# Kernel optimization log

Measured on AMD Instinct MI355X. Metric: run time of the kernel, lower is better.

## Reference

```python
import jax, jax.numpy as jnp
import numpy as np

D_MODEL = 512
N_HEADS = 8
D_HEAD = D_MODEL // N_HEADS
SCALE = D_HEAD ** -0.5


def _rel_shift(x):
    # x: (b, h, qlen, klen) -> Transformer-XL relative shift
    b, h, qlen, klen = x.shape
    x = jnp.pad(x, ((0, 0), (0, 0), (0, 0), (1, 0)))        # (b,h,q,k+1)
    x = x.reshape(b, h, klen + 1, qlen)
    x = x[:, :, 1:, :].reshape(b, h, qlen, klen)
    return x


def setup_inputs() -> dict:
    key = jax.random.key(0)
    ks = jax.random.split(key, 12)
    B, S = 2, 2048
    P = 2 * S - 1
    w = lambda k, shape: (jax.random.normal(k, shape, jnp.float32) * 0.02)
    return {
        "x": jax.random.normal(ks[0], (B, S, D_MODEL), jnp.float32),
        "pos_emb": jax.random.normal(ks[1], (P, D_MODEL), jnp.float32),
        "Wq": w(ks[2], (D_MODEL, D_MODEL)), "bq": jnp.zeros((D_MODEL,), jnp.float32),
        "Wk": w(ks[3], (D_MODEL, D_MODEL)), "bk": jnp.zeros((D_MODEL,), jnp.float32),
        "Wv": w(ks[4], (D_MODEL, D_MODEL)), "bv": jnp.zeros((D_MODEL,), jnp.float32),
        "Wp": w(ks[5], (D_MODEL, D_MODEL)),
        "Wo": w(ks[6], (D_MODEL, D_MODEL)), "bo": jnp.zeros((D_MODEL,), jnp.float32),
        "pos_bias_u": w(ks[7], (N_HEADS, D_HEAD)),
        "pos_bias_v": w(ks[8], (N_HEADS, D_HEAD)),
    }


def reference(x, pos_emb, Wq, bq, Wk, bk, Wv, bv, Wp, Wo, bo, pos_bias_u, pos_bias_v):
    B, S, _ = x.shape
    # projections (torch Linear: y = x @ W^T + b; here W stored as (in, out))
    q = (x @ Wq + bq).reshape(B, S, N_HEADS, D_HEAD)
    k = (x @ Wk + bk).reshape(B, S, N_HEADS, D_HEAD)
    v = (x @ Wv + bv).reshape(B, S, N_HEADS, D_HEAD)
    p = (pos_emb @ Wp).reshape(-1, N_HEADS, D_HEAD)  # (2S-1, H, D)

    # content score: (q + u) @ k^T  -> (B,H,S,S)
    content = jnp.einsum("bshd,bthd->bhst", q + pos_bias_u, k)
    # position score: (q + v_bias) @ p^T -> (B,H,S,2S-1), then rel_shift
    pos = jnp.einsum("bshd,phd->bhsp", q + pos_bias_v, p)
    pos = _rel_shift(pos)[..., :S]  # trim to kv_len

    attn = jax.nn.softmax((content + pos) * SCALE, axis=-1)
    out = jnp.einsum("bhst,bthd->bshd", attn, v).reshape(B, S, D_MODEL)
    out = out @ Wo + bo
    return out
```

## Files before the change

### kernel.cpp

```cpp
#include <hip/hip_runtime.h>

#define DM    512
#define NH    8
#define DH    64
#define SEQ   2048
#define PLEN  4095
#define NB    2
#define NSPLIT 2
#define JSPAN (SEQ / NSPLIT)
#define ATT_SCALE 0.125f

typedef __attribute__((ext_vector_type(8))) _Float16 half8;
typedef __attribute__((ext_vector_type(4))) float   floatx4;

__global__ __launch_bounds__(256)
void prep(const float* __restrict__ x, const float* __restrict__ pe,
          const float* __restrict__ W0, const float* __restrict__ W1,
          const float* __restrict__ W2, const float* __restrict__ W3,
          const float* __restrict__ W4,
          _Float16* __restrict__ x16, _Float16* __restrict__ pe16,
          _Float16* __restrict__ Wt)
{
    __shared__ _Float16 tile[64 * 72];
    const int z = blockIdx.z;
    const int t = threadIdx.x;

    if (z < 2) {
        const float* src = z ? pe : x;
        _Float16* dst = z ? pe16 : x16;
        const long n = z ? (long)PLEN * DM : (long)NB * SEQ * DM;
        const long i = ((long)blockIdx.x * 256 + t) * 8;
        if (i >= n) return;
        float4 f0 = *(const float4*)(src + i);
        float4 f1 = *(const float4*)(src + i + 4);
        half8 o;
        o[0] = (_Float16)f0.x; o[1] = (_Float16)f0.y;
        o[2] = (_Float16)f0.z; o[3] = (_Float16)f0.w;
        o[4] = (_Float16)f1.x; o[5] = (_Float16)f1.y;
        o[6] = (_Float16)f1.z; o[7] = (_Float16)f1.w;
        *(half8*)(dst + i) = o;
        return;
    }
    if (blockIdx.x >= 64) return;
    const int wz = z - 2;
    const float* W = (wz == 0) ? W0 : (wz == 1) ? W1 : (wz == 2) ? W2
                   : (wz == 3) ? W3 : W4;
    _Float16* dst_base = Wt + (size_t)wz * DM * DM;
    const int n0 = (blockIdx.x & 7) * 64, k0 = (blockIdx.x >> 3) * 64;
    {
        const int kr = t >> 2, nch = (t & 3) * 16;
        const float* src = W + (size_t)(k0 + kr) * DM + n0 + nch;
        float4 f0 = *(const float4*)(src + 0);
        float4 f1 = *(const float4*)(src + 4);
        float4 f2 = *(const float4*)(src + 8);
        float4 f3 = *(const float4*)(src + 12);
        _Float16* trow = &tile[kr * 72 + nch];
        trow[0]  = (_Float16)f0.x; trow[1]  = (_Float16)f0.y;
        trow[2]  = (_Float16)f0.z; trow[3]  = (_Float16)f0.w;
        trow[4]  = (_Float16)f1.x; trow[5]  = (_Float16)f1.y;
        trow[6]  = (_Float16)f1.z; trow[7]  = (_Float16)f1.w;
        trow[8]  = (_Float16)f2.x; trow[9]  = (_Float16)f2.y;
        trow[10] = (_Float16)f2.z; trow[11] = (_Float16)f2.w;
        trow[12] = (_Float16)f3.x; trow[13] = (_Float16)f3.y;
        trow[14] = (_Float16)f3.z; trow[15] = (_Float16)f3.w;
    }
    __syncthreads();
    {
        const int nr = t >> 2, kch = (t & 3) * 16;
        half8 o0, o1;
#pragma unroll
        for (int i = 0; i < 8; ++i) o0[i] = tile[(kch + i) * 72 + nr];
#pragma unroll
        for (int i = 0; i < 8; ++i) o1[i] = tile[(kch + 8 + i) * 72 + nr];
        _Float16* dst = dst_base + (size_t)(n0 + nr) * DM + k0 + kch;
        *(half8*)dst = o0;
        *(half8*)(dst + 8) = o1;
    }
}

__global__ __launch_bounds__(256)
void gemm_qkvp(const _Float16* __restrict__ X, const _Float16* __restrict__ Pe,
               const _Float16* __restrict__ Wt,
               const float* __restrict__ bq, const float* __restrict__ bk,
               const float* __restrict__ bv, const float* __restrict__ bu,
               const float* __restrict__ bvb,
               _Float16* __restrict__ qu16, _Float16* __restrict__ qv16,
               _Float16* __restrict__ k16, _Float16* __restrict__ vt16,
               _Float16* __restrict__ p16)
{
    __shared__ _Float16 aS[64 * 72];
    __shared__ _Float16 wS[64 * 72];

    const int t = threadIdx.x;
    const int w = t >> 6, lane = t & 63, quad = lane >> 4, l16 = lane & 15;
    const int z = blockIdx.z;
    const int n0 = blockIdx.x * 64;
    const int m0 = blockIdx.y * 64;
    const int srow = t >> 2, sch = (t & 3) * 16;
    const _Float16* A = (z == 3) ? Pe : X;
    const _Float16* Wz = Wt + (size_t)z * DM * DM;

    floatx4 acc[4];
#pragma unroll
    for (int ct = 0; ct < 4; ++ct) acc[ct] = (floatx4){0.f, 0.f, 0.f, 0.f};

    for (int k0 = 0; k0 < DM; k0 += 64) {
        __syncthreads();
        if (z != 3 || m0 + srow < PLEN) {
            const _Float16* asrc = A + (size_t)(m0 + srow) * DM + k0 + sch;
            *(half8*)&aS[srow * 72 + sch]     = *(const half8*)asrc;
            *(half8*)&aS[srow * 72 + sch + 8] = *(const half8*)(asrc + 8);
        } else {
            half8 zz = {};
            *(half8*)&aS[srow * 72 + sch]     = zz;
            *(half8*)&aS[srow * 72 + sch + 8] = zz;
        }
        {
            const _Float16* wsrc = Wz + (size_t)(n0 + srow) * DM + k0 + sch;
            *(half8*)&wS[srow * 72 + sch]     = *(const half8*)wsrc;
            *(half8*)&wS[srow * 72 + sch + 8] = *(const half8*)(wsrc + 8);
        }
        __syncthreads();
#pragma unroll
        for (int kb = 0; kb < 2; ++kb) {
            half8 af = *(const half8*)&aS[(16 * w + l16) * 72 + kb * 32 + quad * 8];
#pragma unroll
            for (int ct = 0; ct < 4; ++ct) {
                half8 bf = *(const half8*)&wS[(16 * ct + l16) * 72 + kb * 32 + quad * 8];
                acc[ct] = __builtin_amdgcn_mfma_f32_16x16x32_f16(af, bf, acc[ct], 0, 0, 0);
            }
        }
    }

    const int h = n0 >> 6;
    if (z == 0) {
#pragma unroll
        for (int ct = 0; ct < 4; ++ct) {
            const int n = n0 + 16 * ct + l16;
            const float bval = bq[n], uval = bu[n], vval = bvb[n];
#pragma unroll
            for (int r = 0; r < 4; ++r) {
                const int m = m0 + 16 * w + 4 * quad + r;
                const int b = m >> 11, s = m & 2047;
                const size_t dst = ((size_t)((h * NB + b) * SEQ) + s) * DH + (n & 63);
                const float q = acc[ct][r] + bval;
                qu16[dst] = (_Float16)((q + uval) * ATT_SCALE);
                qv16[dst] = (_Float16)((q + vval) * ATT_SCALE);
            }
        }
    } else if (z == 1) {
#pragma unroll
        for (int ct = 0; ct < 4; ++ct) {
            const int n = n0 + 16 * ct + l16;
            const float bval = bk[n];
#pragma unroll
            for (int r = 0; r < 4; ++r) {
                const int m = m0 + 16 * w + 4 * quad + r;
                const int b = m >> 11, s = m & 2047;
                k16[((size_t)((h * NB + b) * SEQ) + s) * DH + (n & 63)] =
                    (_Float16)(acc[ct][r] + bval);
            }
        }
    } else if (z == 2) {
        __syncthreads();
#pragma unroll
        for (int ct = 0; ct < 4; ++ct) {
            const float bval = bv[n0 + 16 * ct + l16];
#pragma unroll
            for (int r = 0; r < 4; ++r)
                aS[(16 * w + 4 * quad + r) * 72 + 16 * ct + l16] =
                    (_Float16)(acc[ct][r] + bval);
        }
        __syncthreads();
        const int b = m0 >> 11, s0 = m0 & 2047;
        const int drow = t >> 2;
        half8 o0, o1;
#pragma unroll
        for (int i = 0; i < 8; ++i) o0[i] = aS[(sch + i) * 72 + drow];
#pragma unroll
        for (int i = 0; i < 8; ++i) o1[i] = aS[(sch + 8 + i) * 72 + drow];
        _Float16* dst = vt16 + ((size_t)((h * NB + b) * DH) + drow) * SEQ + s0 + sch;
        *(half8*)dst = o0;
        *(half8*)(dst + 8) = o1;
    } else {
#pragma unroll
        for (int ct = 0; ct < 4; ++ct) {
            const int n = n0 + 16 * ct + l16;
#pragma unroll
            for (int r = 0; r < 4; ++r) {
                const int m = m0 + 16 * w + 4 * quad + r;
                if (m < PLEN)
                    p16[((size_t)h * PLEN + m) * DH + (n & 63)] = (_Float16)acc[ct][r];
            }
        }
    }
}

__global__ __launch_bounds__(256, 3)
void relattn_mfma(const _Float16* __restrict__ QU,
                  const _Float16* __restrict__ QV,
                  const _Float16* __restrict__ Kp,
                  const _Float16* __restrict__ VT,
                  const _Float16* __restrict__ Pp,
                  float* __restrict__ Opart, float* __restrict__ Lpart)
{
    __shared__ _Float16 kS[64 * 72];
    __shared__ _Float16 pS[128 * 72];
    __shared__ _Float16 vS[64 * 72];
    __shared__ _Float16 tS[64 * 88];

    const int t = threadIdx.x;
    const int w = t >> 6, lane = t & 63, quad = lane >> 4, l16 = lane & 15;
    const int i0 = blockIdx.x * 64;
    const int h = blockIdx.y;
    const int b = blockIdx.z & (NB - 1);
    const int split = blockIdx.z >> 1;
    const size_t hb = (size_t)(h * NB + b);
    const int cbase = 48 - 16 * w;

    half8 qa[2], va[2];
    {
        const _Float16* qrow = QU + (hb * SEQ + i0 + 16 * w + l16) * DH + quad * 8;
        const _Float16* vrow = QV + (hb * SEQ + i0 + 16 * w + l16) * DH + quad * 8;
        qa[0] = *(const half8*)qrow;       qa[1] = *(const half8*)(qrow + 32);
        va[0] = *(const half8*)vrow;       va[1] = *(const half8*)(vrow + 32);
    }

    floatx4 O[4];
    float lsum[4] = {0.f, 0.f, 0.f, 0.f};
#pragma unroll
    for (int ct = 0; ct < 4; ++ct) O[ct] = (floatx4){0.f, 0.f, 0.f, 0.f};

    const int srow = t >> 2, schunk = (t & 3) * 16;
    const int prow = t >> 1, pch = (t & 1) * 32;

    const _Float16* Kbase = Kp + hb * SEQ * DH;
    const _Float16* Vbase = VT + hb * DH * SEQ;
    const _Float16* Pbase = Pp + (size_t)h * PLEN * DH;

    const int jbeg = split * JSPAN, jend = jbeg + JSPAN;
    for (int j0 = jbeg; j0 < jend; j0 += 64) {
        __syncthreads();

        {
            const _Float16* src = Kbase + (size_t)(j0 + srow) * DH + schunk;
            half8 a0 = *(const half8*)src;
            half8 a1 = *(const half8*)(src + 8);
            *(half8*)&kS[srow * 72 + schunk] = a0;
            *(half8*)&kS[srow * 72 + schunk + 8] = a1;
            const _Float16* vsrc = Vbase + (size_t)srow * SEQ + j0 + schunk;
            half8 b0 = *(const half8*)vsrc;
            half8 b1 = *(const half8*)(vsrc + 8);
            *(half8*)&vS[srow * 72 + schunk] = b0;
            *(half8*)&vS[srow * 72 + schunk + 8] = b1;
        }
        {
            const int rbase = (SEQ - 1) + j0 - i0 - 63;
            if (prow < 127) {
                const _Float16* psrc = Pbase + (size_t)(rbase + prow) * DH + pch;
                half8 p0 = *(const half8*)(psrc + 0);
                half8 p1 = *(const half8*)(psrc + 8);
                half8 p2 = *(const half8*)(psrc + 16);
                half8 p3 = *(const half8*)(psrc + 24);
                *(half8*)&pS[prow * 72 + pch + 0]  = p0;
                *(half8*)&pS[prow * 72 + pch + 8]  = p1;
                *(half8*)&pS[prow * 72 + pch + 16] = p2;
                *(half8*)&pS[prow * 72 + pch + 24] = p3;
            }
        }
        __syncthreads();

        floatx4 Tacc[5], Sc[4];
#pragma unroll
        for (int c2 = 0; c2 < 5; ++c2) Tacc[c2] = (floatx4){0.f, 0.f, 0.f, 0.f};
#pragma unroll
        for (int ct = 0; ct < 4; ++ct) Sc[ct] = (floatx4){0.f, 0.f, 0.f, 0.f};
#pragma unroll
        for (int kb = 0; kb < 2; ++kb) {
#pragma unroll
            for (int c2 = 0; c2 < 5; ++c2) {
                half8 bf = *(const half8*)&pS[(cbase + 16 * c2 + l16) * 72 + kb * 32 + quad * 8];
                Tacc[c2] = __builtin_amdgcn_mfma_f32_16x16x32_f16(va[kb], bf, Tacc[c2], 0, 0, 0);
            }
#pragma unroll
            for (int ct = 0; ct < 4; ++ct) {
                half8 bf = *(const half8*)&kS[(16 * ct + l16) * 72 + kb * 32 + quad * 8];
                Sc[ct] = __builtin_amdgcn_mfma_f32_16x16x32_f16(qa[kb], bf, Sc[ct], 0, 0, 0);
            }
        }
#pragma unroll
        for (int c2 = 0; c2 < 5; ++c2)
#pragma unroll
            for (int r = 0; r < 4; ++r)
                tS[(16 * w + 4 * quad + r) * 88 + 16 * c2 + l16] = (_Float16)Tacc[c2][r];
        asm volatile("" ::: "memory");

#pragma unroll
        for (int ct = 0; ct < 4; ++ct)
#pragma unroll
            for (int r = 0; r < 4; ++r) {
                const int il16 = 4 * quad + r;
                const int c = 16 * ct + l16 - il16 + 15;
                const float e = __expf(Sc[ct][r] +
                                       (float)tS[(16 * w + il16) * 88 + c]);
                Sc[ct][r] = e;
                lsum[r] += e;
            }
        asm volatile("" ::: "memory");

#pragma unroll
        for (int ct = 0; ct < 4; ++ct)
#pragma unroll
            for (int r = 0; r < 4; ++r)
                tS[(16 * w + 4 * quad + r) * 88 + 16 * ct + l16] = (_Float16)Sc[ct][r];
        asm volatile("" ::: "memory");

#pragma unroll
        for (int kb = 0; kb < 2; ++kb) {
            half8 af = *(const half8*)&tS[(16 * w + l16) * 88 + kb * 32 + quad * 8];
#pragma unroll
            for (int ct = 0; ct < 4; ++ct) {
                half8 bf = *(const half8*)&vS[(16 * ct + l16) * 72 + kb * 32 + quad * 8];
                O[ct] = __builtin_amdgcn_mfma_f32_16x16x32_f16(af, bf, O[ct], 0, 0, 0);
            }
        }
        asm volatile("" ::: "memory");
    }

#pragma unroll
    for (int r = 0; r < 4; ++r) {
#pragma unroll
        for (int m = 1; m < 16; m <<= 1) lsum[r] += __shfl_xor(lsum[r], m);
        const int row = i0 + 16 * w + 4 * quad + r;
        float* orow = Opart + ((size_t)split * NB * SEQ + b * SEQ + row) * DM + h * DH;
#pragma unroll
        for (int ct = 0; ct < 4; ++ct)
            orow[16 * ct + l16] = O[ct][r];
        if (l16 == 0)
            Lpart[((size_t)split * NH * NB + hb) * SEQ + row] = lsum[r];
    }
}

__global__ __launch_bounds__(256)
void gemm_final(const float* __restrict__ Opart, const float* __restrict__ Lpart,
                const _Float16* __restrict__ Wt, const float* __restrict__ bias,
                float* __restrict__ Out)
{
    __shared__ _Float16 aS[64 * 72];
    __shared__ _Float16 wS[64 * 72];
    __shared__ float invS[8][64];

    const int t = threadIdx.x;
    const int w = t >> 6, lane = t & 63, quad = lane >> 4, l16 = lane & 15;
    const int n0 = blockIdx.x * 64;
    const int m0 = blockIdx.y * 64;
    const int srow = t >> 2, sch = (t & 3) * 16;
    const int b = m0 >> 11, s0 = m0 & 2047;

#pragma unroll
    for (int i = t; i < 512; i += 256) {
        const int hh = i >> 6, rr = i & 63;
        const size_t base = ((size_t)hh * NB + b) * SEQ + s0 + rr;
        const float l = Lpart[base] + Lpart[(size_t)NH * NB * SEQ + base];
        invS[hh][rr] = 1.f / l;
    }

    floatx4 acc[4];
#pragma unroll
    for (int ct = 0; ct < 4; ++ct) acc[ct] = (floatx4){0.f, 0.f, 0.f, 0.f};

    for (int k0 = 0; k0 < DM; k0 += 64) {
        __syncthreads();
        {
            const size_t aoff = ((size_t)b * SEQ + s0 + srow) * DM + k0 + sch;
            const float* a0 = Opart + aoff;
            const float* a1 = Opart + (size_t)NB * SEQ * DM + aoff;
            const float inv = invS[k0 >> 6][srow];
            half8 o0, o1;
#pragma unroll
            for (int c4 = 0; c4 < 2; ++c4) {
                float4 x0 = *(const float4*)(a0 + c4 * 4);
                float4 y0 = *(const float4*)(a1 + c4 * 4);
                o0[c4 * 4 + 0] = (_Float16)((x0.x + y0.x) * inv);
                o0[c4 * 4 + 1] = (_Float16)((x0.y + y0.y) * inv);
                o0[c4 * 4 + 2] = (_Float16)((x0.z + y0.z) * inv);
                o0[c4 * 4 + 3] = (_Float16)((x0.w + y0.w) * inv);
            }
#pragma unroll
            for (int c4 = 0; c4 < 2; ++c4) {
                float4 x0 = *(const float4*)(a0 + 8 + c4 * 4);
                float4 y0 = *(const float4*)(a1 + 8 + c4 * 4);
                o1[c4 * 4 + 0] = (_Float16)((x0.x + y0.x) * inv);
                o1[c4 * 4 + 1] = (_Float16)((x0.y + y0.y) * inv);
                o1[c4 * 4 + 2] = (_Float16)((x0.z + y0.z) * inv);
                o1[c4 * 4 + 3] = (_Float16)((x0.w + y0.w) * inv);
            }
            *(half8*)&aS[srow * 72 + sch]     = o0;
            *(half8*)&aS[srow * 72 + sch + 8] = o1;
            const _Float16* wsrc = Wt + (size_t)(n0 + srow) * DM + k0 + sch;
            *(half8*)&wS[srow * 72 + sch]     = *(const half8*)wsrc;
            *(half8*)&wS[srow * 72 + sch + 8] = *(const half8*)(wsrc + 8);
        }
        __syncthreads();
#pragma unroll
        for (int kb = 0; kb < 2; ++kb) {
            half8 af = *(const half8*)&aS[(16 * w + l16) * 72 + kb * 32 + quad * 8];
#pragma unroll
            for (int ct = 0; ct < 4; ++ct) {
                half8 bf = *(const half8*)&wS[(16 * ct + l16) * 72 + kb * 32 + quad * 8];
                acc[ct] = __builtin_amdgcn_mfma_f32_16x16x32_f16(af, bf, acc[ct], 0, 0, 0);
            }
        }
    }

#pragma unroll
    for (int ct = 0; ct < 4; ++ct) {
        const int n = n0 + 16 * ct + l16;
        const float bval = bias[n];
#pragma unroll
        for (int r = 0; r < 4; ++r) {
            const int m = m0 + 16 * w + 4 * quad + r;
            Out[(size_t)m * DM + n] = acc[ct][r] + bval;
        }
    }
}

extern "C" void kernel_launch(void* const* d_in, const int* in_sizes, int n_in,
                              void* d_out, int out_size, void* d_ws, size_t ws_size,
                              hipStream_t stream)
{
    (void)in_sizes; (void)n_in; (void)out_size; (void)ws_size;
    const float* x   = (const float*)d_in[0];
    const float* pe  = (const float*)d_in[1];
    const float* Wq  = (const float*)d_in[2];
    const float* bq  = (const float*)d_in[3];
    const float* Wk  = (const float*)d_in[4];
    const float* bk  = (const float*)d_in[5];
    const float* Wv  = (const float*)d_in[6];
    const float* bv  = (const float*)d_in[7];
    const float* Wp  = (const float*)d_in[8];
    const float* Wo  = (const float*)d_in[9];
    const float* bo  = (const float*)d_in[10];
    const float* pbu = (const float*)d_in[11];
    const float* pbv = (const float*)d_in[12];
    float* out = (float*)d_out;

    const size_t nX  = (size_t)NB * SEQ * DM;
    const size_t nPe = (size_t)PLEN * DM;
    const size_t nW  = (size_t)DM * DM;
    const size_t nH  = (size_t)NH * NB * SEQ * DH;
    const size_t nPh = (size_t)NH * PLEN * DH;

    _Float16* x16  = (_Float16*)d_ws;
    _Float16* pe16 = x16 + nX;
    _Float16* wt   = pe16 + nPe;
    _Float16* qu16 = wt + 5 * nW;
    _Float16* qv16 = qu16 + nH;
    _Float16* k16  = qv16 + nH;
    _Float16* vt16 = k16 + nH;
    _Float16* p16  = vt16 + nH;
    float* Opart   = (float*)(p16 + nPh);
    float* Lpart   = Opart + (size_t)NSPLIT * NB * SEQ * DM;

    dim3 blk(256);
    prep<<<dim3(1024, 1, 7), blk, 0, stream>>>(x, pe, Wq, Wk, Wv, Wp, Wo,
                                               x16, pe16, wt);
    gemm_qkvp<<<dim3(8, 64, 4), blk, 0, stream>>>(x16, pe16, wt,
                                                  bq, bk, bv, pbu, pbv,
                                                  qu16, qv16, k16, vt16, p16);
    relattn_mfma<<<dim3(SEQ / 64, NH, NB * NSPLIT), blk, 0, stream>>>(
        qu16, qv16, k16, vt16, p16, Opart, Lpart);
    gemm_final<<<dim3(8, 64), blk, 0, stream>>>(Opart, Lpart, wt + 4 * nW, bo,
                                                out);
}
```

Measured before the change: 214.9 us.

## Restructure attention into single-wave blocks reading K/V/P directly from global

The attention kernel now uses one 64-thread wave per 16-query block instead of 256-thread blocks over 64 queries. K, V and P tiles are read straight from global memory into MFMA operands, with no shared-memory staging and no block barriers. Shared memory is used only for a transposed float position-score tile and a swizzled probability tile. Partial outputs are stored as fp16, halving Opart traffic into the final GEMM, at the cost of K/V/P reuse across waves now relying on cache and some precision loss in the partials.

```diff
diff --git a/kernel.cpp b/kernel.cpp
--- a/kernel.cpp
+++ b/kernel.cpp
@@ -6,8 +6,8 @@
 #define SEQ   2048
 #define PLEN  4095
 #define NB    2
-#define NSPLIT 2
-#define JSPAN (SEQ / NSPLIT)
+#define OSPLIT 2
+#define JSPAN (SEQ / OSPLIT)
 #define ATT_SCALE 0.125f
 
 typedef __attribute__((ext_vector_type(8))) _Float16 half8;
@@ -196,32 +196,28 @@
     }
 }
 
-__global__ __launch_bounds__(256, 3)
-void relattn_mfma(const _Float16* __restrict__ QU,
+__global__ __launch_bounds__(64, 4)
+void relattn_wave(const _Float16* __restrict__ QU,
                   const _Float16* __restrict__ QV,
                   const _Float16* __restrict__ Kp,
                   const _Float16* __restrict__ VT,
                   const _Float16* __restrict__ Pp,
-                  float* __restrict__ Opart, float* __restrict__ Lpart)
+                  _Float16* __restrict__ Opart, float* __restrict__ Lpart)
 {
-    __shared__ _Float16 kS[64 * 72];
-    __shared__ _Float16 pS[128 * 72];
-    __shared__ _Float16 vS[64 * 72];
-    __shared__ _Float16 tS[64 * 88];
-
-    const int t = threadIdx.x;
-    const int w = t >> 6, lane = t & 63, quad = lane >> 4, l16 = lane & 15;
-    const int i0 = blockIdx.x * 64;
+    __shared__ float    tT[80 * 20];
+    __shared__ _Float16 bS[16 * 72];
+
+    const int lane = threadIdx.x;
+    const int quad = lane >> 4, l16 = lane & 15;
+    const int i0 = blockIdx.x * 16;
     const int h = blockIdx.y;
-    const int b = blockIdx.z & (NB - 1);
-    const int split = blockIdx.z >> 1;
+    const int b = blockIdx.z & 1, split = blockIdx.z >> 1;
     const size_t hb = (size_t)(h * NB + b);
-    const int cbase = 48 - 16 * w;
 
     half8 qa[2], va[2];
     {
-        const _Float16* qrow = QU + (hb * SEQ + i0 + 16 * w + l16) * DH + quad * 8;
-        const _Float16* vrow = QV + (hb * SEQ + i0 + 16 * w + l16) * DH + quad * 8;
+        const _Float16* qrow = QU + (hb * SEQ + i0 + l16) * DH + quad * 8;
+        const _Float16* vrow = QV + (hb * SEQ + i0 + l16) * DH + quad * 8;
         qa[0] = *(const half8*)qrow;       qa[1] = *(const half8*)(qrow + 32);
         va[0] = *(const half8*)vrow;       va[1] = *(const half8*)(vrow + 32);
     }
@@ -231,118 +227,94 @@
 #pragma unroll
     for (int ct = 0; ct < 4; ++ct) O[ct] = (floatx4){0.f, 0.f, 0.f, 0.f};
 
-    const int srow = t >> 2, schunk = (t & 3) * 16;
-    const int prow = t >> 1, pch = (t & 1) * 32;
-
-    const _Float16* Kbase = Kp + hb * SEQ * DH;
-    const _Float16* Vbase = VT + hb * DH * SEQ;
-    const _Float16* Pbase = Pp + (size_t)h * PLEN * DH;
+    const _Float16* Kb = Kp + hb * SEQ * DH;
+    const _Float16* Vb = VT + hb * DH * SEQ;
+    const _Float16* Pb = Pp + (size_t)h * PLEN * DH;
 
     const int jbeg = split * JSPAN, jend = jbeg + JSPAN;
     for (int j0 = jbeg; j0 < jend; j0 += 64) {
-        __syncthreads();
-
-        {
-            const _Float16* src = Kbase + (size_t)(j0 + srow) * DH + schunk;
-            half8 a0 = *(const half8*)src;
-            half8 a1 = *(const half8*)(src + 8);
-            *(half8*)&kS[srow * 72 + schunk] = a0;
-            *(half8*)&kS[srow * 72 + schunk + 8] = a1;
-            const _Float16* vsrc = Vbase + (size_t)srow * SEQ + j0 + schunk;
-            half8 b0 = *(const half8*)vsrc;
-            half8 b1 = *(const half8*)(vsrc + 8);
-            *(half8*)&vS[srow * 72 + schunk] = b0;
-            *(half8*)&vS[srow * 72 + schunk + 8] = b1;
-        }
-        {
-            const int rbase = (SEQ - 1) + j0 - i0 - 63;
-            if (prow < 127) {
-                const _Float16* psrc = Pbase + (size_t)(rbase + prow) * DH + pch;
-                half8 p0 = *(const half8*)(psrc + 0);
-                half8 p1 = *(const half8*)(psrc + 8);
-                half8 p2 = *(const half8*)(psrc + 16);
-                half8 p3 = *(const half8*)(psrc + 24);
-                *(half8*)&pS[prow * 72 + pch + 0]  = p0;
-                *(half8*)&pS[prow * 72 + pch + 8]  = p1;
-                *(half8*)&pS[prow * 72 + pch + 16] = p2;
-                *(half8*)&pS[prow * 72 + pch + 24] = p3;
-            }
-        }
-        __syncthreads();
-
-        floatx4 Tacc[5], Sc[4];
-#pragma unroll
-        for (int c2 = 0; c2 < 5; ++c2) Tacc[c2] = (floatx4){0.f, 0.f, 0.f, 0.f};
+        const int pbase = (SEQ - 16) + j0 - i0;
+
+        floatx4 Tc[5], Sc[4];
+#pragma unroll
+        for (int c2 = 0; c2 < 5; ++c2) Tc[c2] = (floatx4){0.f, 0.f, 0.f, 0.f};
 #pragma unroll
         for (int ct = 0; ct < 4; ++ct) Sc[ct] = (floatx4){0.f, 0.f, 0.f, 0.f};
 #pragma unroll
         for (int kb = 0; kb < 2; ++kb) {
 #pragma unroll
             for (int c2 = 0; c2 < 5; ++c2) {
-                half8 bf = *(const half8*)&pS[(cbase + 16 * c2 + l16) * 72 + kb * 32 + quad * 8];
-                Tacc[c2] = __builtin_amdgcn_mfma_f32_16x16x32_f16(va[kb], bf, Tacc[c2], 0, 0, 0);
+                int prow = pbase + 16 * c2 + l16;
+                if (prow > PLEN - 1) prow = PLEN - 1;
+                half8 bf = *(const half8*)(Pb + (size_t)prow * DH + kb * 32 + quad * 8);
+                Tc[c2] = __builtin_amdgcn_mfma_f32_16x16x32_f16(va[kb], bf, Tc[c2], 0, 0, 0);
             }
 #pragma unroll
             for (int ct = 0; ct < 4; ++ct) {
-                half8 bf = *(const half8*)&kS[(16 * ct + l16) * 72 + kb * 32 + quad * 8];
+                half8 bf = *(const half8*)(Kb + (size_t)(j0 + 16 * ct + l16) * DH + kb * 32 + quad * 8);
                 Sc[ct] = __builtin_amdgcn_mfma_f32_16x16x32_f16(qa[kb], bf, Sc[ct], 0, 0, 0);
             }
         }
-#pragma unroll
-        for (int c2 = 0; c2 < 5; ++c2)
-#pragma unroll
-            for (int r = 0; r < 4; ++r)
-                tS[(16 * w + 4 * quad + r) * 88 + 16 * c2 + l16] = (_Float16)Tacc[c2][r];
+
+#pragma unroll
+        for (int c2 = 0; c2 < 5; ++c2) {
+            const int c = 16 * c2 + l16;
+            const int ibase = (4 * quad + 4 * c) & 15;
+            *(floatx4*)&tT[20 * c + ibase] = Tc[c2];
+        }
         asm volatile("" ::: "memory");
 
 #pragma unroll
         for (int ct = 0; ct < 4; ++ct)
 #pragma unroll
             for (int r = 0; r < 4; ++r) {
-                const int il16 = 4 * quad + r;
-                const int c = 16 * ct + l16 - il16 + 15;
-                const float e = __expf(Sc[ct][r] +
-                                       (float)tS[(16 * w + il16) * 88 + c]);
+                const int il = 4 * quad + r;
+                const int c = 16 * ct + l16 - il + 15;
+                const float tval = tT[20 * c + ((il + 4 * c) & 15)];
+                const float e = __expf(Sc[ct][r] + tval);
                 Sc[ct][r] = e;
                 lsum[r] += e;
             }
         asm volatile("" ::: "memory");
 
 #pragma unroll
+        for (int ct = 0; ct < 4; ++ct) {
+            const int col = 16 * ct + l16;
+            const int cjs = ((col >> 3) ^ quad) * 8 + (col & 7);
+#pragma unroll
+            for (int r = 0; r < 4; ++r)
+                bS[(4 * quad + r) * 72 + cjs] = (_Float16)Sc[ct][r];
+        }
+        asm volatile("" ::: "memory");
+
+#pragma unroll
+        for (int kb = 0; kb < 2; ++kb) {
+            half8 af = *(const half8*)&bS[l16 * 72 + ((4 * kb + quad) ^ (l16 >> 2)) * 8];
+#pragma unroll
+            for (int ct = 0; ct < 4; ++ct) {
+                half8 bf = *(const half8*)(Vb + (size_t)(16 * ct + l16) * SEQ + j0 + kb * 32 + quad * 8);
+                O[ct] = __builtin_amdgcn_mfma_f32_16x16x32_f16(af, bf, O[ct], 0, 0, 0);
+            }
+        }
+        asm volatile("" ::: "memory");
+    }
+
+#pragma unroll
+    for (int r = 0; r < 4; ++r) {
+#pragma unroll
+        for (int m = 1; m < 16; m <<= 1) lsum[r] += __shfl_xor(lsum[r], m);
+        const int s = i0 + 4 * quad + r;
+        _Float16* orow = Opart + ((size_t)(split * NB + b) * SEQ + s) * DM + h * DH;
+#pragma unroll
         for (int ct = 0; ct < 4; ++ct)
-#pragma unroll
-            for (int r = 0; r < 4; ++r)
-                tS[(16 * w + 4 * quad + r) * 88 + 16 * ct + l16] = (_Float16)Sc[ct][r];
-        asm volatile("" ::: "memory");
-
-#pragma unroll
-        for (int kb = 0; kb < 2; ++kb) {
-            half8 af = *(const half8*)&tS[(16 * w + l16) * 88 + kb * 32 + quad * 8];
-#pragma unroll
-            for (int ct = 0; ct < 4; ++ct) {
-                half8 bf = *(const half8*)&vS[(16 * ct + l16) * 72 + kb * 32 + quad * 8];
-                O[ct] = __builtin_amdgcn_mfma_f32_16x16x32_f16(af, bf, O[ct], 0, 0, 0);
-            }
-        }
-        asm volatile("" ::: "memory");
-    }
-
-#pragma unroll
-    for (int r = 0; r < 4; ++r) {
-#pragma unroll
-        for (int m = 1; m < 16; m <<= 1) lsum[r] += __shfl_xor(lsum[r], m);
-        const int row = i0 + 16 * w + 4 * quad + r;
-        float* orow = Opart + ((size_t)split * NB * SEQ + b * SEQ + row) * DM + h * DH;
-#pragma unroll
-        for (int ct = 0; ct < 4; ++ct)
-            orow[16 * ct + l16] = O[ct][r];
+            orow[16 * ct + l16] = (_Float16)O[ct][r];
         if (l16 == 0)
-            Lpart[((size_t)split * NH * NB + hb) * SEQ + row] = lsum[r];
+            Lpart[((size_t)split * NH * NB + hb) * SEQ + s] = lsum[r];
     }
 }
 
 __global__ __launch_bounds__(256)
-void gemm_final(const float* __restrict__ Opart, const float* __restrict__ Lpart,
+void gemm_final(const _Float16* __restrict__ Opart, const float* __restrict__ Lpart,
                 const _Float16* __restrict__ Wt, const float* __restrict__ bias,
                 float* __restrict__ Out)
 {
@@ -373,28 +345,20 @@
         __syncthreads();
         {
             const size_t aoff = ((size_t)b * SEQ + s0 + srow) * DM + k0 + sch;
-            const float* a0 = Opart + aoff;
-            const float* a1 = Opart + (size_t)NB * SEQ * DM + aoff;
+            const _Float16* a0 = Opart + aoff;
+            const _Float16* a1 = Opart + (size_t)NB * SEQ * DM + aoff;
             const float inv = invS[k0 >> 6][srow];
+            half8 x0 = *(const half8*)a0;
+            half8 x1 = *(const half8*)(a0 + 8);
+            half8 y0 = *(const half8*)a1;
+            half8 y1 = *(const half8*)(a1 + 8);
             half8 o0, o1;
 #pragma unroll
-            for (int c4 = 0; c4 < 2; ++c4) {
-                float4 x0 = *(const float4*)(a0 + c4 * 4);
-                float4 y0 = *(const float4*)(a1 + c4 * 4);
-                o0[c4 * 4 + 0] = (_Float16)((x0.x + y0.x) * inv);
-                o0[c4 * 4 + 1] = (_Float16)((x0.y + y0.y) * inv);
-                o0[c4 * 4 + 2] = (_Float16)((x0.z + y0.z) * inv);
-                o0[c4 * 4 + 3] = (_Float16)((x0.w + y0.w) * inv);
-            }
-#pragma unroll
-            for (int c4 = 0; c4 < 2; ++c4) {
-                float4 x0 = *(const float4*)(a0 + 8 + c4 * 4);
-                float4 y0 = *(const float4*)(a1 + 8 + c4 * 4);
-                o1[c4 * 4 + 0] = (_Float16)((x0.x + y0.x) * inv);
-                o1[c4 * 4 + 1] = (_Float16)((x0.y + y0.y) * inv);
-                o1[c4 * 4 + 2] = (_Float16)((x0.z + y0.z) * inv);
-                o1[c4 * 4 + 3] = (_Float16)((x0.w + y0.w) * inv);
-            }
+            for (int i = 0; i < 8; ++i)
+                o0[i] = (_Float16)(((float)x0[i] + (float)y0[i]) * inv);
+#pragma unroll
+            for (int i = 0; i < 8; ++i)
+                o1[i] = (_Float16)(((float)x1[i] + (float)y1[i]) * inv);
             *(half8*)&aS[srow * 72 + sch]     = o0;
             *(half8*)&aS[srow * 72 + sch + 8] = o1;
             const _Float16* wsrc = Wt + (size_t)(n0 + srow) * DM + k0 + sch;
@@ -459,8 +423,8 @@
     _Float16* k16  = qv16 + nH;
     _Float16* vt16 = k16 + nH;
     _Float16* p16  = vt16 + nH;
-    float* Opart   = (float*)(p16 + nPh);
-    float* Lpart   = Opart + (size_t)NSPLIT * NB * SEQ * DM;
+    _Float16* Opart = p16 + nPh + 64;
+    float* Lpart    = (float*)(Opart + (size_t)OSPLIT * NB * SEQ * DM);
 
     dim3 blk(256);
     prep<<<dim3(1024, 1, 7), blk, 0, stream>>>(x, pe, Wq, Wk, Wv, Wp, Wo,
@@ -468,7 +432,7 @@
     gemm_qkvp<<<dim3(8, 64, 4), blk, 0, stream>>>(x16, pe16, wt,
                                                   bq, bk, bv, pbu, pbv,
                                                   qu16, qv16, k16, vt16, p16);
-    relattn_mfma<<<dim3(SEQ / 64, NH, NB * NSPLIT), blk, 0, stream>>>(
+    relattn_wave<<<dim3(SEQ / 16, NH, NB * OSPLIT), dim3(64), 0, stream>>>(
         qu16, qv16, k16, vt16, p16, Opart, Lpart);
     gemm_final<<<dim3(8, 64), blk, 0, stream>>>(Opart, Lpart, wt + 4 * nW, bo,
                                                 out);
```

Result: slower. 318.3 us (+48.1%).

## Register-prefetch next tiles, drop KV split, normalize attention output in-kernel

Applied to the files above, without the earlier changes.

Removes the two-way split over the key dimension, so each attention block covers the full sequence and writes normalized fp16 output directly. This drops the fp32 partial buffers and the combine step in the output GEMM. The GEMMs and the attention loop now prefetch the next tile into registers while the current tile is computed. Occupancy hint drops from 3 to 2 blocks per CU to make room for the prefetch registers. The grid halves to 512 blocks, which reduces parallelism, and the projection GEMM now clamps out-of-range rows instead of zero-filling them.

```diff
diff --git a/kernel.cpp b/kernel.cpp
--- a/kernel.cpp
+++ b/kernel.cpp
@@ -6,8 +6,6 @@
 #define SEQ   2048
 #define PLEN  4095
 #define NB    2
-#define NSPLIT 2
-#define JSPAN (SEQ / NSPLIT)
 #define ATT_SCALE 0.125f
 
 typedef __attribute__((ext_vector_type(8))) _Float16 half8;
@@ -100,27 +98,33 @@
     const _Float16* A = (z == 3) ? Pe : X;
     const _Float16* Wz = Wt + (size_t)z * DM * DM;
 
+    int arow = m0 + srow;
+    if (z == 3 && arow > PLEN - 1) arow = PLEN - 1;
+    const _Float16* arowp = A + (size_t)arow * DM + sch;
+    const _Float16* wrowp = Wz + (size_t)(n0 + srow) * DM + sch;
+
     floatx4 acc[4];
 #pragma unroll
     for (int ct = 0; ct < 4; ++ct) acc[ct] = (floatx4){0.f, 0.f, 0.f, 0.f};
 
+    half8 pa0 = *(const half8*)arowp;
+    half8 pa1 = *(const half8*)(arowp + 8);
+    half8 pw0 = *(const half8*)wrowp;
+    half8 pw1 = *(const half8*)(wrowp + 8);
+
     for (int k0 = 0; k0 < DM; k0 += 64) {
         __syncthreads();
-        if (z != 3 || m0 + srow < PLEN) {
-            const _Float16* asrc = A + (size_t)(m0 + srow) * DM + k0 + sch;
-            *(half8*)&aS[srow * 72 + sch]     = *(const half8*)asrc;
-            *(half8*)&aS[srow * 72 + sch + 8] = *(const half8*)(asrc + 8);
-        } else {
-            half8 zz = {};
-            *(half8*)&aS[srow * 72 + sch]     = zz;
-            *(half8*)&aS[srow * 72 + sch + 8] = zz;
-        }
-        {
-            const _Float16* wsrc = Wz + (size_t)(n0 + srow) * DM + k0 + sch;
-            *(half8*)&wS[srow * 72 + sch]     = *(const half8*)wsrc;
-            *(half8*)&wS[srow * 72 + sch + 8] = *(const half8*)(wsrc + 8);
-        }
-        __syncthreads();
+        *(half8*)&aS[srow * 72 + sch]     = pa0;
+        *(half8*)&aS[srow * 72 + sch + 8] = pa1;
+        *(half8*)&wS[srow * 72 + sch]     = pw0;
+        *(half8*)&wS[srow * 72 + sch + 8] = pw1;
+        __syncthreads();
+        if (k0 + 64 < DM) {
+            pa0 = *(const half8*)(arowp + k0 + 64);
+            pa1 = *(const half8*)(arowp + k0 + 72);
+            pw0 = *(const half8*)(wrowp + k0 + 64);
+            pw1 = *(const half8*)(wrowp + k0 + 72);
+        }
 #pragma unroll
         for (int kb = 0; kb < 2; ++kb) {
             half8 af = *(const half8*)&aS[(16 * w + l16) * 72 + kb * 32 + quad * 8];
@@ -196,13 +200,13 @@
     }
 }
 
-__global__ __launch_bounds__(256, 3)
+__global__ __launch_bounds__(256, 2)
 void relattn_mfma(const _Float16* __restrict__ QU,
                   const _Float16* __restrict__ QV,
                   const _Float16* __restrict__ Kp,
                   const _Float16* __restrict__ VT,
                   const _Float16* __restrict__ Pp,
-                  float* __restrict__ Opart, float* __restrict__ Lpart)
+                  _Float16* __restrict__ Out)
 {
     __shared__ _Float16 kS[64 * 72];
     __shared__ _Float16 pS[128 * 72];
@@ -212,9 +216,7 @@
     const int t = threadIdx.x;
     const int w = t >> 6, lane = t & 63, quad = lane >> 4, l16 = lane & 15;
     const int i0 = blockIdx.x * 64;
-    const int h = blockIdx.y;
-    const int b = blockIdx.z & (NB - 1);
-    const int split = blockIdx.z >> 1;
+    const int h = blockIdx.y, b = blockIdx.z;
     const size_t hb = (size_t)(h * NB + b);
     const int cbase = 48 - 16 * w;
 
@@ -237,64 +239,88 @@
     const _Float16* Kbase = Kp + hb * SEQ * DH;
     const _Float16* Vbase = VT + hb * DH * SEQ;
     const _Float16* Pbase = Pp + (size_t)h * PLEN * DH;
-
-    const int jbeg = split * JSPAN, jend = jbeg + JSPAN;
-    for (int j0 = jbeg; j0 < jend; j0 += 64) {
-        __syncthreads();
+    const int rbase0 = (SEQ - 1) - i0 - 63;
+
+    half8 pk0, pk1, pv0, pv1;
+    half8 pp0 = {}, pp1 = {}, pp2 = {}, pp3 = {};
+    {
+        const _Float16* src = Kbase + (size_t)srow * DH + schunk;
+        pk0 = *(const half8*)src;
+        pk1 = *(const half8*)(src + 8);
+        const _Float16* vsrc = Vbase + (size_t)srow * SEQ + schunk;
+        pv0 = *(const half8*)vsrc;
+        pv1 = *(const half8*)(vsrc + 8);
+        if (prow < 127) {
+            const _Float16* psrc = Pbase + (size_t)(rbase0 + prow) * DH + pch;
+            pp0 = *(const half8*)(psrc + 0);
+            pp1 = *(const half8*)(psrc + 8);
+            pp2 = *(const half8*)(psrc + 16);
+            pp3 = *(const half8*)(psrc + 24);
+        }
+    }
+
+    for (int j0 = 0; j0 < SEQ; j0 += 64) {
+        __syncthreads();
+
+        *(half8*)&kS[srow * 72 + schunk]     = pk0;
+        *(half8*)&kS[srow * 72 + schunk + 8] = pk1;
+        *(half8*)&vS[srow * 72 + schunk]     = pv0;
+        *(half8*)&vS[srow * 72 + schunk + 8] = pv1;
+        if (prow < 127) {
+            *(half8*)&pS[prow * 72 + pch + 0]  = pp0;
+            *(half8*)&pS[prow * 72 + pch + 8]  = pp1;
+            *(half8*)&pS[prow * 72 + pch + 16] = pp2;
+            *(half8*)&pS[prow * 72 + pch + 24] = pp3;
+        }
+        __syncthreads();
+
+        if (j0 + 64 < SEQ) {
+            const _Float16* src = Kbase + (size_t)(j0 + 64 + srow) * DH + schunk;
+            pk0 = *(const half8*)src;
+            pk1 = *(const half8*)(src + 8);
+            const _Float16* vsrc = Vbase + (size_t)srow * SEQ + j0 + 64 + schunk;
+            pv0 = *(const half8*)vsrc;
+            pv1 = *(const half8*)(vsrc + 8);
+            if (prow < 127) {
+                const _Float16* psrc = Pbase + (size_t)(rbase0 + j0 + 64 + prow) * DH + pch;
+                pp0 = *(const half8*)(psrc + 0);
+                pp1 = *(const half8*)(psrc + 8);
+                pp2 = *(const half8*)(psrc + 16);
+                pp3 = *(const half8*)(psrc + 24);
+            }
+        }
 
         {
-            const _Float16* src = Kbase + (size_t)(j0 + srow) * DH + schunk;
-            half8 a0 = *(const half8*)src;
-            half8 a1 = *(const half8*)(src + 8);
-            *(half8*)&kS[srow * 72 + schunk] = a0;
-            *(half8*)&kS[srow * 72 + schunk + 8] = a1;
-            const _Float16* vsrc = Vbase + (size_t)srow * SEQ + j0 + schunk;
-            half8 b0 = *(const half8*)vsrc;
-            half8 b1 = *(const half8*)(vsrc + 8);
-            *(half8*)&vS[srow * 72 + schunk] = b0;
-            *(half8*)&vS[srow * 72 + schunk + 8] = b1;
-        }
-        {
-            const int rbase = (SEQ - 1) + j0 - i0 - 63;
-            if (prow < 127) {
-                const _Float16* psrc = Pbase + (size_t)(rbase + prow) * DH + pch;
-                half8 p0 = *(const half8*)(psrc + 0);
-                half8 p1 = *(const half8*)(psrc + 8);
-                half8 p2 = *(const half8*)(psrc + 16);
-                half8 p3 = *(const half8*)(psrc + 24);
-                *(half8*)&pS[prow * 72 + pch + 0]  = p0;
-                *(half8*)&pS[prow * 72 + pch + 8]  = p1;
-                *(half8*)&pS[prow * 72 + pch + 16] = p2;
-                *(half8*)&pS[prow * 72 + pch + 24] = p3;
-            }
-        }
-        __syncthreads();
-
-        floatx4 Tacc[5], Sc[4];
-#pragma unroll
-        for (int c2 = 0; c2 < 5; ++c2) Tacc[c2] = (floatx4){0.f, 0.f, 0.f, 0.f};
+            floatx4 Tacc[5];
+#pragma unroll
+            for (int c2 = 0; c2 < 5; ++c2) Tacc[c2] = (floatx4){0.f, 0.f, 0.f, 0.f};
+#pragma unroll
+            for (int kb = 0; kb < 2; ++kb) {
+#pragma unroll
+                for (int c2 = 0; c2 < 5; ++c2) {
+                    half8 bf = *(const half8*)&pS[(cbase + 16 * c2 + l16) * 72 + kb * 32 + quad * 8];
+                    Tacc[c2] = __builtin_amdgcn_mfma_f32_16x16x32_f16(va[kb], bf, Tacc[c2], 0, 0, 0);
+                }
+            }
+#pragma unroll
+            for (int c2 = 0; c2 < 5; ++c2)
+#pragma unroll
+                for (int r = 0; r < 4; ++r)
+                    tS[(16 * w + 4 * quad + r) * 88 + 16 * c2 + l16] = (_Float16)Tacc[c2][r];
+        }
+        asm volatile("" ::: "memory");
+
+        floatx4 Sc[4];
 #pragma unroll
         for (int ct = 0; ct < 4; ++ct) Sc[ct] = (floatx4){0.f, 0.f, 0.f, 0.f};
 #pragma unroll
         for (int kb = 0; kb < 2; ++kb) {
-#pragma unroll
-            for (int c2 = 0; c2 < 5; ++c2) {
-                half8 bf = *(const half8*)&pS[(cbase + 16 * c2 + l16) * 72 + kb * 32 + quad * 8];
-                Tacc[c2] = __builtin_amdgcn_mfma_f32_16x16x32_f16(va[kb], bf, Tacc[c2], 0, 0, 0);
-            }
 #pragma unroll
             for (int ct = 0; ct < 4; ++ct) {
                 half8 bf = *(const half8*)&kS[(16 * ct + l16) * 72 + kb * 32 + quad * 8];
                 Sc[ct] = __builtin_amdgcn_mfma_f32_16x16x32_f16(qa[kb], bf, Sc[ct], 0, 0, 0);
             }
         }
-#pragma unroll
-        for (int c2 = 0; c2 < 5; ++c2)
-#pragma unroll
-            for (int r = 0; r < 4; ++r)
-                tS[(16 * w + 4 * quad + r) * 88 + 16 * c2 + l16] = (_Float16)Tacc[c2][r];
-        asm volatile("" ::: "memory");
-
 #pragma unroll
         for (int ct = 0; ct < 4; ++ct)
 #pragma unroll
@@ -331,77 +357,52 @@
     for (int r = 0; r < 4; ++r) {
 #pragma unroll
         for (int m = 1; m < 16; m <<= 1) lsum[r] += __shfl_xor(lsum[r], m);
-        const int row = i0 + 16 * w + 4 * quad + r;
-        float* orow = Opart + ((size_t)split * NB * SEQ + b * SEQ + row) * DM + h * DH;
+        const float inv = 1.f / lsum[r];
+        _Float16* orow = Out + (size_t)(b * SEQ + i0 + 16 * w + 4 * quad + r) * DM + h * DH;
 #pragma unroll
         for (int ct = 0; ct < 4; ++ct)
-            orow[16 * ct + l16] = O[ct][r];
-        if (l16 == 0)
-            Lpart[((size_t)split * NH * NB + hb) * SEQ + row] = lsum[r];
+            orow[16 * ct + l16] = (_Float16)(O[ct][r] * inv);
     }
 }
 
 __global__ __launch_bounds__(256)
-void gemm_final(const float* __restrict__ Opart, const float* __restrict__ Lpart,
-                const _Float16* __restrict__ Wt, const float* __restrict__ bias,
-                float* __restrict__ Out)
+void gemm_out(const _Float16* __restrict__ A, const _Float16* __restrict__ Wt,
+              const float* __restrict__ bias, float* __restrict__ Out)
 {
     __shared__ _Float16 aS[64 * 72];
     __shared__ _Float16 wS[64 * 72];
-    __shared__ float invS[8][64];
 
     const int t = threadIdx.x;
     const int w = t >> 6, lane = t & 63, quad = lane >> 4, l16 = lane & 15;
     const int n0 = blockIdx.x * 64;
     const int m0 = blockIdx.y * 64;
     const int srow = t >> 2, sch = (t & 3) * 16;
-    const int b = m0 >> 11, s0 = m0 & 2047;
-
-#pragma unroll
-    for (int i = t; i < 512; i += 256) {
-        const int hh = i >> 6, rr = i & 63;
-        const size_t base = ((size_t)hh * NB + b) * SEQ + s0 + rr;
-        const float l = Lpart[base] + Lpart[(size_t)NH * NB * SEQ + base];
-        invS[hh][rr] = 1.f / l;
-    }
+
+    const _Float16* arowp = A + (size_t)(m0 + srow) * DM + sch;
+    const _Float16* wrowp = Wt + (size_t)(n0 + srow) * DM + sch;
 
     floatx4 acc[4];
 #pragma unroll
     for (int ct = 0; ct < 4; ++ct) acc[ct] = (floatx4){0.f, 0.f, 0.f, 0.f};
 
+    half8 pa0 = *(const half8*)arowp;
+    half8 pa1 = *(const half8*)(arowp + 8);
+    half8 pw0 = *(const half8*)wrowp;
+    half8 pw1 = *(const half8*)(wrowp + 8);
+
     for (int k0 = 0; k0 < DM; k0 += 64) {
         __syncthreads();
-        {
-            const size_t aoff = ((size_t)b * SEQ + s0 + srow) * DM + k0 + sch;
-            const float* a0 = Opart + aoff;
-            const float* a1 = Opart + (size_t)NB * SEQ * DM + aoff;
-            const float inv = invS[k0 >> 6][srow];
-            half8 o0, o1;
-#pragma unroll
-            for (int c4 = 0; c4 < 2; ++c4) {
-                float4 x0 = *(const float4*)(a0 + c4 * 4);
-                float4 y0 = *(const float4*)(a1 + c4 * 4);
-                o0[c4 * 4 + 0] = (_Float16)((x0.x + y0.x) * inv);
-                o0[c4 * 4 + 1] = (_Float16)((x0.y + y0.y) * inv);
-                o0[c4 * 4 + 2] = (_Float16)((x0.z + y0.z) * inv);
-                o0[c4 * 4 + 3] = (_Float16)((x0.w + y0.w) * inv);
-            }
-#pragma unroll
-            for (int c4 = 0; c4 < 2; ++c4) {
-                float4 x0 = *(const float4*)(a0 + 8 + c4 * 4);
-                float4 y0 = *(const float4*)(a1 + 8 + c4 * 4);
-                o1[c4 * 4 + 0] = (_Float16)((x0.x + y0.x) * inv);
-                o1[c4 * 4 + 1] = (_Float16)((x0.y + y0.y) * inv);
-                o1[c4 * 4 + 2] = (_Float16)((x0.z + y0.z) * inv);
-                o1[c4 * 4 + 3] = (_Float16)((x0.w + y0.w) * inv);
-            }
-            *(half8*)&aS[srow * 72 + sch]     = o0;
-            *(half8*)&aS[srow * 72 + sch + 8] = o1;
-            const _Float16* wsrc = Wt + (size_t)(n0 + srow) * DM + k0 + sch;
-            *(half8*)&wS[srow * 72 + sch]     = *(const half8*)wsrc;
-            *(half8*)&wS[srow * 72 + sch + 8] = *(const half8*)(wsrc + 8);
-        }
-        __syncthreads();
+        *(half8*)&aS[srow * 72 + sch]     = pa0;
+        *(half8*)&aS[srow * 72 + sch + 8] = pa1;
+        *(half8*)&wS[srow * 72 + sch]     = pw0;
+        *(half8*)&wS[srow * 72 + sch + 8] = pw1;
+        __syncthreads();
+        if (k0 + 64 < DM) {
+            pa0 = *(const half8*)(arowp + k0 + 64);
+            pa1 = *(const half8*)(arowp + k0 + 72);
+            pw0 = *(const half8*)(wrowp + k0 + 64);
+            pw1 = *(const half8*)(wrowp + k0 + 72);
+        }
 #pragma unroll
         for (int kb = 0; kb < 2; ++kb) {
             half8 af = *(const half8*)&aS[(16 * w + l16) * 72 + kb * 32 + quad * 8];
@@ -459,8 +460,7 @@
     _Float16* k16  = qv16 + nH;
     _Float16* vt16 = k16 + nH;
     _Float16* p16  = vt16 + nH;
-    float* Opart   = (float*)(p16 + nPh);
-    float* Lpart   = Opart + (size_t)NSPLIT * NB * SEQ * DM;
+    _Float16* ow16 = p16 + nPh;
 
     dim3 blk(256);
     prep<<<dim3(1024, 1, 7), blk, 0, stream>>>(x, pe, Wq, Wk, Wv, Wp, Wo,
@@ -468,8 +468,7 @@
     gemm_qkvp<<<dim3(8, 64, 4), blk, 0, stream>>>(x16, pe16, wt,
                                                   bq, bk, bv, pbu, pbv,
                                                   qu16, qv16, k16, vt16, p16);
-    relattn_mfma<<<dim3(SEQ / 64, NH, NB * NSPLIT), blk, 0, stream>>>(
-        qu16, qv16, k16, vt16, p16, Opart, Lpart);
-    gemm_final<<<dim3(8, 64), blk, 0, stream>>>(Opart, Lpart, wt + 4 * nW, bo,
-                                                out);
+    relattn_mfma<<<dim3(SEQ / 64, NH, NB), blk, 0, stream>>>(
+        qu16, qv16, k16, vt16, p16, ow16);
+    gemm_out<<<dim3(8, 64), blk, 0, stream>>>(ow16, wt + 4 * nW, bo, out);
 }
```

Measured after the change: 187.0 us. 1.15x faster.
